# Optimization experiments

Hardware: AMD Instinct MI355X
Metric: run time of the kernel (lower is better)

## Reference

```python
import jax, jax.numpy as jnp
import numpy as np

N_NODES = 50000
N_EDGES = 800000
F_IN = 128
HID = 128
F_EDGE = 16
F_TAB = 16
N_CLASSES = 3
BN_EPS = 1e-5


def setup_inputs() -> dict:
    key = jax.random.key(0)
    ks = jax.random.split(key, 20)
    s = lambda *sh: 1.0 / np.sqrt(sh[0])
    inp = {
        "x": jax.random.normal(ks[0], (N_NODES, F_IN), jnp.float32),
        "edge_index": jax.random.randint(ks[1], (2, N_EDGES), 0, N_NODES, jnp.int32),
        "edge_attr": jax.random.normal(ks[2], (N_EDGES, F_EDGE), jnp.float32),
        "tabular_features": jax.random.normal(ks[3], (N_EDGES, F_TAB), jnp.float32),
        # SAGEConv1: lin_l (aggregated neighbors, with bias) + lin_r (root, no bias)
        "W1l": jax.random.normal(ks[4], (F_IN, HID), jnp.float32) * s(F_IN),
        "b1l": jnp.zeros((HID,), jnp.float32),
        "W1r": jax.random.normal(ks[5], (F_IN, HID), jnp.float32) * s(F_IN),
        # SAGEConv2
        "W2l": jax.random.normal(ks[6], (HID, HID), jnp.float32) * s(HID),
        "b2l": jnp.zeros((HID,), jnp.float32),
        "W2r": jax.random.normal(ks[7], (HID, HID), jnp.float32) * s(HID),
        # BatchNorm params / running stats (eval mode)
        "g1": jnp.ones((HID,), jnp.float32), "be1": jnp.zeros((HID,), jnp.float32),
        "m1": jnp.zeros((HID,), jnp.float32), "v1": jnp.ones((HID,), jnp.float32),
        "g2": jnp.ones((HID,), jnp.float32), "be2": jnp.zeros((HID,), jnp.float32),
        "m2": jnp.zeros((HID,), jnp.float32), "v2": jnp.ones((HID,), jnp.float32),
        # Classifier MLP: (2*HID + F_EDGE + F_TAB) -> 128 -> 64 -> 3
        "Wc1": jax.random.normal(ks[8], (2 * HID + F_EDGE + F_TAB, 128), jnp.float32) * s(2 * HID + F_EDGE + F_TAB),
        "bc1": jnp.zeros((128,), jnp.float32),
        "Wc2": jax.random.normal(ks[9], (128, 64), jnp.float32) * s(128),
        "bc2": jnp.zeros((64,), jnp.float32),
        "Wc3": jax.random.normal(ks[10], (64, N_CLASSES), jnp.float32) * s(64),
        "bc3": jnp.zeros((N_CLASSES,), jnp.float32),
    }
    return inp


def _sage(x, src, dst, Wl, bl, Wr):
    # PyG SAGEConv (mean aggr): out_i = lin_l(mean_{j->i} x_j) + lin_r(x_i)
    msg = x[src]                                            # [E, F] gather
    agg = jax.ops.segment_sum(msg, dst, num_segments=N_NODES)
    cnt = jax.ops.segment_sum(jnp.ones((src.shape[0],), x.dtype), dst, num_segments=N_NODES)
    agg = agg / jnp.maximum(cnt, 1.0)[:, None]
    return agg @ Wl + bl + x @ Wr


def _bn(h, g, b, m, v):
    return (h - m) * (g * jax.lax.rsqrt(v + BN_EPS)) + b


def reference(x, edge_index, edge_attr, tabular_features,
              W1l, b1l, W1r, W2l, b2l, W2r,
              g1, be1, m1, v1, g2, be2, m2, v2,
              Wc1, bc1, Wc2, bc2, Wc3, bc3):
    src, dst = edge_index[0], edge_index[1]
    h = jax.nn.relu(_bn(_sage(x, src, dst, W1l, b1l, W1r), g1, be1, m1, v1))
    h = jax.nn.relu(_bn(_sage(h, src, dst, W2l, b2l, W2r), g2, be2, m2, v2))
    # eval mode: dropout is identity
    edge_repr = jnp.concatenate([h[src], h[dst], edge_attr, tabular_features], axis=-1)  # [E, 288]
    z = jax.nn.relu(edge_repr @ Wc1 + bc1)
    z = jax.nn.relu(z @ Wc2 + bc2)
    return z @ Wc3 + bc3  # [E, num_classes]
```

## Files before the change

### kernel.cpp

```cpp
#include <hip/hip_runtime.h>
#include <stdint.h>

#define NHID 128
#define EPB 64
#define RP  296
#define Z1P 136
#define Z2P 72

typedef _Float16 half8 __attribute__((ext_vector_type(8)));
typedef _Float16 half4v __attribute__((ext_vector_type(4)));
typedef float f32x4 __attribute__((ext_vector_type(4)));

__global__ void zero_kernel(float* __restrict__ p, size_t n4) {
    size_t i = (size_t)blockIdx.x * blockDim.x + threadIdx.x;
    size_t stride = (size_t)gridDim.x * blockDim.x;
    float4* p4 = (float4*)p;
    float4 z = make_float4(0.f, 0.f, 0.f, 0.f);
    for (size_t j = i; j < n4; j += stride) p4[j] = z;
}

__global__ void cast_f32_f16(const float* __restrict__ in, _Float16* __restrict__ outp,
                             int n8) {
    int i = blockIdx.x * 256 + threadIdx.x;
    int stride = gridDim.x * 256;
    for (int j = i; j < n8; j += stride) {
        float4 a = ((const float4*)in)[2 * j];
        float4 b = ((const float4*)in)[2 * j + 1];
        half8 v;
        v[0] = (_Float16)a.x; v[1] = (_Float16)a.y; v[2] = (_Float16)a.z; v[3] = (_Float16)a.w;
        v[4] = (_Float16)b.x; v[5] = (_Float16)b.y; v[6] = (_Float16)b.z; v[7] = (_Float16)b.w;
        ((half8*)outp)[j] = v;
    }
}

__global__ void prep_weights(const float* __restrict__ Wc1, const float* __restrict__ Wc2,
                             const float* __restrict__ Wc3,
                             const float* __restrict__ W1l, const float* __restrict__ W1r,
                             const float* __restrict__ W2l, const float* __restrict__ W2r,
                             _Float16* __restrict__ W1T, _Float16* __restrict__ W2T,
                             _Float16* __restrict__ W3T,
                             _Float16* __restrict__ WT1, _Float16* __restrict__ WT2) {
    int tid = blockIdx.x * 256 + threadIdx.x;
    if (tid < 288 * 128) {
        int n = tid / 288, k = tid % 288;
        W1T[tid] = (_Float16)Wc1[(size_t)k * 128 + n];
    }
    if (tid < 64 * 128) {
        int n = tid / 128, k = tid % 128;
        W2T[tid] = (_Float16)Wc2[(size_t)k * 64 + n];
    }
    if (tid < 16 * 64) {
        int n = tid / 64, k = tid % 64;
        W3T[tid] = (n < 3) ? (_Float16)Wc3[(size_t)k * 3 + n] : (_Float16)0.f;
    }
    if (tid < 128 * 256) {
        int n = tid / 256, k = tid % 256;
        WT1[tid] = (k < 128) ? (_Float16)W1l[(size_t)k * 128 + n]
                             : (_Float16)W1r[(size_t)(k - 128) * 128 + n];
        WT2[tid] = (k < 128) ? (_Float16)W2l[(size_t)k * 128 + n]
                             : (_Float16)W2r[(size_t)(k - 128) * 128 + n];
    }
}

__global__ void count_kernel(const int* __restrict__ dst, int* __restrict__ deg, int E) {
    int e = blockIdx.x * 256 + threadIdx.x;
    if (e < E) atomicAdd(&deg[dst[e]], 1);
}

__global__ __launch_bounds__(256) void csr_reduce(const int* __restrict__ deg,
                                                  int* __restrict__ bsum, int N) {
    __shared__ int b[256];
    int t = threadIdx.x;
    int i = blockIdx.x * 256 + t;
    int v = (i < N) ? deg[i] : 0;
    b[t] = v;
    __syncthreads();
#pragma unroll
    for (int off = 128; off > 0; off >>= 1) {
        if (t < off) b[t] += b[t + off];
        __syncthreads();
    }
    if (t == 0) bsum[blockIdx.x] = b[0];
}

__global__ __launch_bounds__(256) void csr_scan_partials(const int* __restrict__ bsum,
                                                         int* __restrict__ bpre,
                                                         int* __restrict__ rowptr,
                                                         int nb, int N) {
    __shared__ int b[256];
    int t = threadIdx.x;
    int v = (t < nb) ? bsum[t] : 0;
    b[t] = v;
    __syncthreads();
    int x = v;
#pragma unroll
    for (int off = 1; off < 256; off <<= 1) {
        int y = (t >= off) ? b[t - off] : 0;
        __syncthreads();
        x += y;
        b[t] = x;
        __syncthreads();
    }
    if (t < nb) bpre[t] = x - v;
    if (t == nb - 1) rowptr[N] = x;
}

__global__ __launch_bounds__(256) void csr_emit(const int* __restrict__ deg,
                                                const int* __restrict__ bpre,
                                                int* __restrict__ rowptr,
                                                int* __restrict__ cursor, int N) {
    __shared__ int b[256];
    int t = threadIdx.x;
    int i = blockIdx.x * 256 + t;
    int v = (i < N) ? deg[i] : 0;
    b[t] = v;
    __syncthreads();
    int x = v;
#pragma unroll
    for (int off = 1; off < 256; off <<= 1) {
        int y = (t >= off) ? b[t - off] : 0;
        __syncthreads();
        x += y;
        b[t] = x;
        __syncthreads();
    }
    if (i < N) {
        int excl = bpre[blockIdx.x] + x - v;
        rowptr[i] = excl;
        cursor[i] = excl;
    }
}

__global__ void fill_kernel(const int* __restrict__ src, const int* __restrict__ dst,
                            int* __restrict__ cursor, int* __restrict__ ssrc, int E) {
    int e = blockIdx.x * 256 + threadIdx.x;
    if (e < E) {
        int p = atomicAdd(&cursor[dst[e]], 1);
        ssrc[p] = src[e];
    }
}

__global__ __launch_bounds__(512) void sage_layer(
    const _Float16* __restrict__ xin, const int* __restrict__ rowptr,
    const int* __restrict__ ssrc,
    const _Float16* __restrict__ WT, const float* __restrict__ bl,
    const float* __restrict__ gam, const float* __restrict__ bet,
    const float* __restrict__ mu, const float* __restrict__ var,
    _Float16* __restrict__ outp, int N) {
    __shared__ _Float16 sAX[16][264];
    int tid = threadIdx.x;
    int node0 = blockIdx.x * 16;

    {
        int i = tid >> 5;
        int q = tid & 31;
        int node = node0 + i;
        int rs = rowptr[node], re = rowptr[node + 1];
        float4 acc = make_float4(0.f, 0.f, 0.f, 0.f);
        int e = rs;
        for (; e + 4 <= re; e += 4) {
            int s0 = ssrc[e], s1 = ssrc[e + 1], s2 = ssrc[e + 2], s3 = ssrc[e + 3];
            half4v v0 = *(const half4v*)&xin[(size_t)s0 * NHID + q * 4];
            half4v v1 = *(const half4v*)&xin[(size_t)s1 * NHID + q * 4];
            half4v v2 = *(const half4v*)&xin[(size_t)s2 * NHID + q * 4];
            half4v v3 = *(const half4v*)&xin[(size_t)s3 * NHID + q * 4];
            acc.x += ((float)v0[0] + (float)v1[0]) + ((float)v2[0] + (float)v3[0]);
            acc.y += ((float)v0[1] + (float)v1[1]) + ((float)v2[1] + (float)v3[1]);
            acc.z += ((float)v0[2] + (float)v1[2]) + ((float)v2[2] + (float)v3[2]);
            acc.w += ((float)v0[3] + (float)v1[3]) + ((float)v2[3] + (float)v3[3]);
        }
        for (; e < re; e++) {
            half4v v = *(const half4v*)&xin[(size_t)ssrc[e] * NHID + q * 4];
            acc.x += (float)v[0]; acc.y += (float)v[1];
            acc.z += (float)v[2]; acc.w += (float)v[3];
        }
        int deg = re - rs;
        float inv = (deg > 0) ? (1.0f / (float)deg) : 0.f;
        half4v av;
        av[0] = (_Float16)(acc.x * inv); av[1] = (_Float16)(acc.y * inv);
        av[2] = (_Float16)(acc.z * inv); av[3] = (_Float16)(acc.w * inv);
        *(half4v*)&sAX[i][q * 4] = av;
        *(half4v*)&sAX[i][128 + q * 4] = *(const half4v*)&xin[(size_t)node * NHID + q * 4];
    }
    __syncthreads();

    {
        int lane = tid & 63;
        int wave = tid >> 6;
        int l15 = lane & 15;
        int g = lane >> 4;
        const _Float16* wb = WT + (size_t)(wave * 16 + l15) * 256 + g * 8;
        f32x4 acc = (f32x4){0.f, 0.f, 0.f, 0.f};
#pragma unroll
        for (int kt = 0; kt < 8; kt++) {
            half8 af = *(const half8*)&sAX[l15][kt * 32 + g * 8];
            half8 bf = *(const half8*)(wb + kt * 32);
            acc = __builtin_amdgcn_mfma_f32_16x16x32_f16(af, bf, acc, 0, 0, 0);
        }
        int o = wave * 16 + l15;
        float scale = gam[o] * rsqrtf(var[o] + 1e-5f);
        float bias = bet[o];
        float mean = mu[o];
        float bb = bl[o];
#pragma unroll
        for (int r = 0; r < 4; r++) {
            float hv = acc[r] + bb;
            hv = (hv - mean) * scale + bias;
            hv = fmaxf(hv, 0.f);
            outp[(size_t)(node0 + g * 4 + r) * NHID + o] = (_Float16)hv;
        }
    }
}

__global__ __launch_bounds__(256, 1) void classifier_mfma(
    const _Float16* __restrict__ h2f, const int* __restrict__ src,
    const int* __restrict__ dst,
    const float* __restrict__ attr, const float* __restrict__ tab,
    const _Float16* __restrict__ W1T, const float* __restrict__ bc1,
    const _Float16* __restrict__ W2T, const float* __restrict__ bc2,
    const _Float16* __restrict__ W3T, const float* __restrict__ bc3,
    float* __restrict__ out, int E, int ntiles) {
    __shared__ _Float16 repr[EPB][RP];
    __shared__ _Float16 z1s[EPB][Z1P];
    _Float16* z2f = &repr[0][0];

    int tid = threadIdx.x;
    int lane = tid & 63;
    int wave = tid >> 6;
    int l15 = lane & 15;
    int g = lane >> 4;

    half8 B1[2][9];
#pragma unroll
    for (int nn = 0; nn < 2; nn++) {
        const _Float16* wb = W1T + (size_t)((2 * wave + nn) * 16 + l15) * 288 + g * 8;
#pragma unroll
        for (int kt = 0; kt < 9; kt++) B1[nn][kt] = *(const half8*)(wb + kt * 32);
    }
    float4 bias1v[2];
#pragma unroll
    for (int nn = 0; nn < 2; nn++)
        bias1v[nn] = *(const float4*)&bc1[(2 * wave + nn) * 16 + g * 4];
    half8 B2[4];
    const _Float16* w2base = W2T + (size_t)(wave * 16 + l15) * 128 + g * 8;
#pragma unroll
    for (int kt = 0; kt < 4; kt++) B2[kt] = *(const half8*)(w2base + kt * 32);
    float4 bias2v = *(const float4*)&bc2[wave * 16 + g * 4];
    half8 B3[2];
#pragma unroll
    for (int kt = 0; kt < 2; kt++)
        B3[kt] = *(const half8*)(W3T + (size_t)l15 * 64 + kt * 32 + g * 8);
    float b3_0 = bc3[0], b3_1 = bc3[1], b3_2 = bc3[2];

    for (int t = blockIdx.x; t < ntiles; t += gridDim.x) {
        int e0 = t * EPB;
        {
            int el = tid >> 2, p = tid & 3;
            int e = e0 + el; if (e >= E) e = E - 1;
            int s = src[e], d = dst[e];
            const half8* hs = (const half8*)(h2f + (size_t)s * NHID + p * 32);
            const half8* hd = (const half8*)(h2f + (size_t)d * NHID + p * 32);
            half8* r = (half8*)&repr[el][0];
#pragma unroll
            for (int j = 0; j < 4; j++) r[p * 4 + j] = hs[j];
#pragma unroll
            for (int j = 0; j < 4; j++) r[16 + p * 4 + j] = hd[j];
            const float* ssrcp = (p < 2) ? (attr + (size_t)e * 16 + p * 8)
                                         : (tab + (size_t)e * 16 + (p - 2) * 8);
            int doff = (p < 2) ? (32 + p) : (34 + (p - 2));
            float4 a = ((const float4*)ssrcp)[0], b = ((const float4*)ssrcp)[1];
            half8 v;
            v[0] = (_Float16)a.x; v[1] = (_Float16)a.y; v[2] = (_Float16)a.z; v[3] = (_Float16)a.w;
            v[4] = (_Float16)b.x; v[5] = (_Float16)b.y; v[6] = (_Float16)b.z; v[7] = (_Float16)b.w;
            r[doff] = v;
        }
        __syncthreads();

#pragma unroll
        for (int at = 0; at < 4; at++) {
            const _Float16* ab = &repr[at * 16 + l15][g * 8];
            f32x4 acc0 = (f32x4){bias1v[0].x, bias1v[0].y, bias1v[0].z, bias1v[0].w};
            f32x4 acc1 = (f32x4){bias1v[1].x, bias1v[1].y, bias1v[1].z, bias1v[1].w};
#pragma unroll
            for (int kt = 0; kt < 9; kt++) {
                half8 af = *(const half8*)(ab + kt * 32);
                acc0 = __builtin_amdgcn_mfma_f32_16x16x32_f16(B1[0][kt], af, acc0, 0, 0, 0);
                acc1 = __builtin_amdgcn_mfma_f32_16x16x32_f16(B1[1][kt], af, acc1, 0, 0, 0);
            }
            half4v p0, p1;
#pragma unroll
            for (int r = 0; r < 4; r++) {
                p0[r] = (_Float16)fmaxf(acc0[r], 0.f);
                p1[r] = (_Float16)fmaxf(acc1[r], 0.f);
            }
            *(half4v*)&z1s[at * 16 + l15][(2 * wave + 0) * 16 + g * 4] = p0;
            *(half4v*)&z1s[at * 16 + l15][(2 * wave + 1) * 16 + g * 4] = p1;
        }
        __syncthreads();

#pragma unroll
        for (int a = 0; a < 4; a++) {
            const _Float16* ab = &z1s[a * 16 + l15][g * 8];
            f32x4 acc2 = (f32x4){bias2v.x, bias2v.y, bias2v.z, bias2v.w};
#pragma unroll
            for (int kt = 0; kt < 4; kt++)
                acc2 = __builtin_amdgcn_mfma_f32_16x16x32_f16(B2[kt], *(const half8*)(ab + kt * 32),
                                                              acc2, 0, 0, 0);
            half4v p;
#pragma unroll
            for (int r = 0; r < 4; r++) p[r] = (_Float16)fmaxf(acc2[r], 0.f);
            *(half4v*)&z2f[(size_t)(a * 16 + l15) * Z2P + wave * 16 + g * 4] = p;
        }
        __syncthreads();

        {
            const _Float16* ab = z2f + (size_t)(wave * 16 + l15) * Z2P + g * 8;
            f32x4 acc3 = (f32x4){0.f, 0.f, 0.f, 0.f};
#pragma unroll
            for (int kt = 0; kt < 2; kt++)
                acc3 = __builtin_amdgcn_mfma_f32_16x16x32_f16(B3[kt], *(const half8*)(ab + kt * 32),
                                                              acc3, 0, 0, 0);
            if (g == 0) {
                int e = e0 + wave * 16 + l15;
                if (e < E) {
                    out[(size_t)e * 3 + 0] = acc3[0] + b3_0;
                    out[(size_t)e * 3 + 1] = acc3[1] + b3_1;
                    out[(size_t)e * 3 + 2] = acc3[2] + b3_2;
                }
            }
        }
        __syncthreads();
    }
}

extern "C" void kernel_launch(void* const* d_in, const int* in_sizes, int n_in,
                              void* d_out, int out_size, void* d_ws, size_t ws_size,
                              hipStream_t stream) {
    const float* x    = (const float*)d_in[0];
    const int*   ei   = (const int*)d_in[1];
    const float* attr = (const float*)d_in[2];
    const float* tab  = (const float*)d_in[3];
    const float* W1l  = (const float*)d_in[4];
    const float* b1l  = (const float*)d_in[5];
    const float* W1r  = (const float*)d_in[6];
    const float* W2l  = (const float*)d_in[7];
    const float* b2l  = (const float*)d_in[8];
    const float* W2r  = (const float*)d_in[9];
    const float* g1   = (const float*)d_in[10];
    const float* be1  = (const float*)d_in[11];
    const float* m1   = (const float*)d_in[12];
    const float* v1   = (const float*)d_in[13];
    const float* g2   = (const float*)d_in[14];
    const float* be2  = (const float*)d_in[15];
    const float* m2   = (const float*)d_in[16];
    const float* v2   = (const float*)d_in[17];
    const float* Wc1  = (const float*)d_in[18];
    const float* bc1  = (const float*)d_in[19];
    const float* Wc2  = (const float*)d_in[20];
    const float* bc2  = (const float*)d_in[21];
    const float* Wc3  = (const float*)d_in[22];
    const float* bc3  = (const float*)d_in[23];
    float* out = (float*)d_out;

    const int N = in_sizes[0] / NHID;
    const int E = in_sizes[1] / 2;

    char* ws = (char*)d_ws;
    int*       rowptr = (int*)(ws + 0);
    int*       cursor = (int*)(ws + 204800);
    int*       deg    = (int*)(ws + 409600);
    int*       ssrc   = (int*)(ws + 614400);
    int*       bsum   = (int*)(ws + 3814400);
    int*       bpre   = (int*)(ws + 3815424);
    _Float16*  W1T    = (_Float16*)(ws + 3816448);
    _Float16*  W2T    = (_Float16*)(ws + 3890176);
    _Float16*  W3T    = (_Float16*)(ws + 3906560);
    _Float16*  WT1    = (_Float16*)(ws + 3908608);
    _Float16*  WT2    = (_Float16*)(ws + 3974144);
    _Float16*  xf     = (_Float16*)(ws + 4039680);
    _Float16*  h1f    = (_Float16*)(ws + 4039680 + (size_t)N * NHID * 2);
    _Float16*  h2f    = (_Float16*)(ws + 4039680 + 2 * (size_t)N * NHID * 2);

    const int* src = ei;
    const int* dst = ei + E;

    int eblocks = (E + 255) / 256;
    int cblocks = (N + 255) / 256;
    int nblocks16 = (N + 15) / 16;
    int ntiles  = (E + EPB - 1) / EPB;
    int cgrid   = 512;
    if (cgrid > ntiles) cgrid = ntiles;
    int n8      = N * NHID / 8;

    prep_weights<<<144, 256, 0, stream>>>(Wc1, Wc2, Wc3, W1l, W1r, W2l, W2r,
                                          W1T, W2T, W3T, WT1, WT2);
    cast_f32_f16<<<1024, 256, 0, stream>>>(x, xf, n8);
    zero_kernel<<<16, 256, 0, stream>>>((float*)deg, 204800 / 16);
    count_kernel<<<eblocks, 256, 0, stream>>>(dst, deg, E);
    csr_reduce<<<cblocks, 256, 0, stream>>>(deg, bsum, N);
    csr_scan_partials<<<1, 256, 0, stream>>>(bsum, bpre, rowptr, cblocks, N);
    csr_emit<<<cblocks, 256, 0, stream>>>(deg, bpre, rowptr, cursor, N);
    fill_kernel<<<eblocks, 256, 0, stream>>>(src, dst, cursor, ssrc, E);
    sage_layer<<<nblocks16, 512, 0, stream>>>(xf, rowptr, ssrc, WT1, b1l,
                                              g1, be1, m1, v1, h1f, N);
    sage_layer<<<nblocks16, 512, 0, stream>>>(h1f, rowptr, ssrc, WT2, b2l,
                                              g2, be2, m2, v2, h2f, N);
    classifier_mfma<<<cgrid, 256, 0, stream>>>(h2f, src, dst, attr, tab,
                                               W1T, bc1, W2T, bc2, W3T, bc3,
                                               out, E, ntiles);
}
```

Baseline: 310.7 us.

## Prefetch next classifier tile during layer-3 MMA; widen SAGE gather to half8 with two teams

The SAGE aggregation now splits each node's 32 threads into two teams of 16. Each thread loads 8 halves, the teams take alternating edges, and a shuffle combines the two partial sums. In the classifier, z2 moves to its own shared buffer, so the next tile's edge representation can be staged into repr before the final MMA stage runs. This hides part of the gather latency behind compute. The cost is extra shared memory, which may reduce occupancy, and a redundant restage of the last tile.

```diff
diff --git a/kernel.cpp b/kernel.cpp
--- a/kernel.cpp
+++ b/kernel.cpp
@@ -153,34 +153,42 @@
 
     {
         int i = tid >> 5;
-        int q = tid & 31;
+        int lsub = tid & 31;
+        int q16 = lsub & 15;
+        int team = lsub >> 4;
         int node = node0 + i;
         int rs = rowptr[node], re = rowptr[node + 1];
-        float4 acc = make_float4(0.f, 0.f, 0.f, 0.f);
-        int e = rs;
-        for (; e + 4 <= re; e += 4) {
-            int s0 = ssrc[e], s1 = ssrc[e + 1], s2 = ssrc[e + 2], s3 = ssrc[e + 3];
-            half4v v0 = *(const half4v*)&xin[(size_t)s0 * NHID + q * 4];
-            half4v v1 = *(const half4v*)&xin[(size_t)s1 * NHID + q * 4];
-            half4v v2 = *(const half4v*)&xin[(size_t)s2 * NHID + q * 4];
-            half4v v3 = *(const half4v*)&xin[(size_t)s3 * NHID + q * 4];
-            acc.x += ((float)v0[0] + (float)v1[0]) + ((float)v2[0] + (float)v3[0]);
-            acc.y += ((float)v0[1] + (float)v1[1]) + ((float)v2[1] + (float)v3[1]);
-            acc.z += ((float)v0[2] + (float)v1[2]) + ((float)v2[2] + (float)v3[2]);
-            acc.w += ((float)v0[3] + (float)v1[3]) + ((float)v2[3] + (float)v3[3]);
-        }
-        for (; e < re; e++) {
-            half4v v = *(const half4v*)&xin[(size_t)ssrc[e] * NHID + q * 4];
-            acc.x += (float)v[0]; acc.y += (float)v[1];
-            acc.z += (float)v[2]; acc.w += (float)v[3];
-        }
+        float acc[8];
+#pragma unroll
+        for (int c = 0; c < 8; c++) acc[c] = 0.f;
+        int e = rs + team;
+        for (; e + 6 < re; e += 8) {
+            int s0 = ssrc[e], s1 = ssrc[e + 2], s2 = ssrc[e + 4], s3 = ssrc[e + 6];
+            half8 v0 = *(const half8*)&xin[(size_t)s0 * NHID + q16 * 8];
+            half8 v1 = *(const half8*)&xin[(size_t)s1 * NHID + q16 * 8];
+            half8 v2 = *(const half8*)&xin[(size_t)s2 * NHID + q16 * 8];
+            half8 v3 = *(const half8*)&xin[(size_t)s3 * NHID + q16 * 8];
+#pragma unroll
+            for (int c = 0; c < 8; c++)
+                acc[c] += ((float)v0[c] + (float)v1[c]) + ((float)v2[c] + (float)v3[c]);
+        }
+        for (; e < re; e += 2) {
+            half8 v = *(const half8*)&xin[(size_t)ssrc[e] * NHID + q16 * 8];
+#pragma unroll
+            for (int c = 0; c < 8; c++) acc[c] += (float)v[c];
+        }
+#pragma unroll
+        for (int c = 0; c < 8; c++) acc[c] += __shfl_xor(acc[c], 16);
         int deg = re - rs;
         float inv = (deg > 0) ? (1.0f / (float)deg) : 0.f;
-        half4v av;
-        av[0] = (_Float16)(acc.x * inv); av[1] = (_Float16)(acc.y * inv);
-        av[2] = (_Float16)(acc.z * inv); av[3] = (_Float16)(acc.w * inv);
-        *(half4v*)&sAX[i][q * 4] = av;
-        *(half4v*)&sAX[i][128 + q * 4] = *(const half4v*)&xin[(size_t)node * NHID + q * 4];
+        if (team == 0) {
+            half8 av;
+#pragma unroll
+            for (int c = 0; c < 8; c++) av[c] = (_Float16)(acc[c] * inv);
+            *(half8*)&sAX[i][q16 * 8] = av;
+            *(half8*)&sAX[i][128 + q16 * 8] =
+                *(const half8*)&xin[(size_t)node * NHID + q16 * 8];
+        }
     }
     __syncthreads();
 
@@ -222,7 +230,7 @@
     float* __restrict__ out, int E, int ntiles) {
     __shared__ _Float16 repr[EPB][RP];
     __shared__ _Float16 z1s[EPB][Z1P];
-    _Float16* z2f = &repr[0][0];
+    __shared__ _Float16 z2s[EPB][Z2P];
 
     int tid = threadIdx.x;
     int lane = tid & 63;
@@ -252,29 +260,33 @@
         B3[kt] = *(const half8*)(W3T + (size_t)l15 * 64 + kt * 32 + g * 8);
     float b3_0 = bc3[0], b3_1 = bc3[1], b3_2 = bc3[2];
 
-    for (int t = blockIdx.x; t < ntiles; t += gridDim.x) {
+    auto STAGE = [&](int tp) {
+        int el = tid >> 2, p = tid & 3;
+        int e = tp * EPB + el; if (e >= E) e = E - 1;
+        int s = src[e], d = dst[e];
+        const half8* hs = (const half8*)(h2f + (size_t)s * NHID + p * 32);
+        const half8* hd = (const half8*)(h2f + (size_t)d * NHID + p * 32);
+        half8* r = (half8*)&repr[el][0];
+#pragma unroll
+        for (int j = 0; j < 4; j++) r[p * 4 + j] = hs[j];
+#pragma unroll
+        for (int j = 0; j < 4; j++) r[16 + p * 4 + j] = hd[j];
+        const float* ssrcp = (p < 2) ? (attr + (size_t)e * 16 + p * 8)
+                                     : (tab + (size_t)e * 16 + (p - 2) * 8);
+        int doff = (p < 2) ? (32 + p) : (34 + (p - 2));
+        float4 a = ((const float4*)ssrcp)[0], b = ((const float4*)ssrcp)[1];
+        half8 v;
+        v[0] = (_Float16)a.x; v[1] = (_Float16)a.y; v[2] = (_Float16)a.z; v[3] = (_Float16)a.w;
+        v[4] = (_Float16)b.x; v[5] = (_Float16)b.y; v[6] = (_Float16)b.z; v[7] = (_Float16)b.w;
+        r[doff] = v;
+    };
+
+    int gd = gridDim.x;
+    STAGE(blockIdx.x);
+    __syncthreads();
+
+    for (int t = blockIdx.x; t < ntiles; t += gd) {
         int e0 = t * EPB;
-        {
-            int el = tid >> 2, p = tid & 3;
-            int e = e0 + el; if (e >= E) e = E - 1;
-            int s = src[e], d = dst[e];
-            const half8* hs = (const half8*)(h2f + (size_t)s * NHID + p * 32);
-            const half8* hd = (const half8*)(h2f + (size_t)d * NHID + p * 32);
-            half8* r = (half8*)&repr[el][0];
-#pragma unroll
-            for (int j = 0; j < 4; j++) r[p * 4 + j] = hs[j];
-#pragma unroll
-            for (int j = 0; j < 4; j++) r[16 + p * 4 + j] = hd[j];
-            const float* ssrcp = (p < 2) ? (attr + (size_t)e * 16 + p * 8)
-                                         : (tab + (size_t)e * 16 + (p - 2) * 8);
-            int doff = (p < 2) ? (32 + p) : (34 + (p - 2));
-            float4 a = ((const float4*)ssrcp)[0], b = ((const float4*)ssrcp)[1];
-            half8 v;
-            v[0] = (_Float16)a.x; v[1] = (_Float16)a.y; v[2] = (_Float16)a.z; v[3] = (_Float16)a.w;
-            v[4] = (_Float16)b.x; v[5] = (_Float16)b.y; v[6] = (_Float16)b.z; v[7] = (_Float16)b.w;
-            r[doff] = v;
-        }
-        __syncthreads();
 
 #pragma unroll
         for (int at = 0; at < 4; at++) {
@@ -309,12 +321,16 @@
             half4v p;
 #pragma unroll
             for (int r = 0; r < 4; r++) p[r] = (_Float16)fmaxf(acc2[r], 0.f);
-            *(half4v*)&z2f[(size_t)(a * 16 + l15) * Z2P + wave * 16 + g * 4] = p;
+            *(half4v*)&z2s[a * 16 + l15][wave * 16 + g * 4] = p;
         }
         __syncthreads();
 
         {
-            const _Float16* ab = z2f + (size_t)(wave * 16 + l15) * Z2P + g * 8;
+            int tp = t + gd; if (tp >= ntiles) tp = t;
+            STAGE(tp);
+        }
+        {
+            const _Float16* ab = &z2s[wave * 16 + l15][g * 8];
             f32x4 acc3 = (f32x4){0.f, 0.f, 0.f, 0.f};
 #pragma unroll
             for (int kt = 0; kt < 2; kt++)
```

Measured after the change: 306.6 us. About the same (-1.3%).
